# Kernel optimization log

Measured on AMD Instinct MI355X. Metric: run time of the kernel, lower is better.

## Reference

```python
import jax, jax.numpy as jnp
import numpy as np

B, IN, OUT = 1024, 512, 64000
EPS = 1e-12  # matches torch F.normalize eps


def setup_inputs() -> dict:
    key = jax.random.key(0)
    k1, k2, k3 = jax.random.split(key, 3)
    x = jax.random.normal(k1, (B, IN), dtype=jnp.float32)
    label = jax.random.randint(k2, (B,), 0, OUT)
    # xavier_uniform_ for weight [OUT, IN]: limit = sqrt(6 / (fan_in + fan_out))
    limit = float(np.sqrt(6.0 / (IN + OUT)))
    weight = jax.random.uniform(k3, (OUT, IN), dtype=jnp.float32, minval=-limit, maxval=limit)
    s = 50               # python scalar; set via _calculate_para but UNUSED in normfree output
    m = jnp.full((1,), 0.5, dtype=jnp.float32)  # margin
    return {"x": x, "label": label, "weight": weight, "s": s, "m": m}


def reference(x, label, weight, s, m):
    m = m.reshape(())
    cos_m, sin_m = jnp.cos(m), jnp.sin(m)
    # norm of raw input (the 'normfree' scale replacing s)
    norm = jnp.linalg.norm(x, axis=1, keepdims=True)            # [B, 1]
    xn = x / jnp.maximum(norm, EPS)                             # F.normalize(input)
    wn = weight / jnp.maximum(
        jnp.linalg.norm(weight, axis=1, keepdims=True), EPS)    # F.normalize(weight)
    cosine = xn @ wn.T                                          # [B, OUT]
    sine = jnp.sqrt(jnp.clip(1.0 - cosine * cosine, 0.0, None))
    phi = cosine * cos_m - sine * sin_m                         # cos(theta + m)
    # per-sample loop in torch == one-hot substitution only where cosine > 0
    onehot = jax.nn.one_hot(label, OUT, dtype=bool)             # [B, OUT]
    mod_cosine = jnp.where(onehot & (cosine > 0), phi, cosine)
    return norm * mod_cosine, wn
```

## Files before the change

### kernel.cpp

```cpp
#include <hip/hip_runtime.h>
#include <cstdint>

#define EPSN 1e-12f
static constexpr int B_ROWS = 1024;
static constexpr int IN_DIM = 512;
static constexpr int OUT_DIM = 64000;

typedef __attribute__((ext_vector_type(8))) short bf16x8;
typedef __attribute__((ext_vector_type(4))) float f32x4;

__device__ __forceinline__ unsigned short f2bf(float f) {
  uint32_t u = __builtin_bit_cast(uint32_t, f);
  u += 0x7fffu + ((u >> 16) & 1u);
  return (unsigned short)(u >> 16);
}

__device__ __forceinline__ float wave_sum(float v) {
#pragma unroll
  for (int off = 32; off; off >>= 1) v += __shfl_xor(v, off);
  return v;
}

__device__ __forceinline__ void async16(const void* g, void* l) {
  __builtin_amdgcn_global_load_lds((const __attribute__((address_space(1))) uint32_t*)g,
                                   (__attribute__((address_space(3))) uint32_t*)l, 16, 0, 0);
}

__global__ void wnorm_kernel(const float* __restrict__ Wg, float* __restrict__ wnOut,
                             unsigned short* __restrict__ wbf, int useBf) {
  int lane = threadIdx.x & 63;
  int row = blockIdx.x * 4 + (threadIdx.x >> 6);
  const float* src = Wg + (size_t)row * IN_DIM + lane * 8;
  float4 a = *(const float4*)src;
  float4 b = *(const float4*)(src + 4);
  float ss = a.x * a.x;
  ss = fmaf(a.y, a.y, ss); ss = fmaf(a.z, a.z, ss); ss = fmaf(a.w, a.w, ss);
  ss = fmaf(b.x, b.x, ss); ss = fmaf(b.y, b.y, ss); ss = fmaf(b.z, b.z, ss);
  ss = fmaf(b.w, b.w, ss);
  ss = wave_sum(ss);
  float inv = 1.0f / fmaxf(sqrtf(ss), EPSN);
  float4 wa, wb;
  wa.x = a.x * inv; wa.y = a.y * inv; wa.z = a.z * inv; wa.w = a.w * inv;
  wb.x = b.x * inv; wb.y = b.y * inv; wb.z = b.z * inv; wb.w = b.w * inv;
  float* dst = wnOut + (size_t)row * IN_DIM + lane * 8;
  *(float4*)dst = wa;
  *(float4*)(dst + 4) = wb;
  if (useBf) {
    uint4 u;
    u.x = (uint32_t)f2bf(wa.x) | ((uint32_t)f2bf(wa.y) << 16);
    u.y = (uint32_t)f2bf(wa.z) | ((uint32_t)f2bf(wa.w) << 16);
    u.z = (uint32_t)f2bf(wb.x) | ((uint32_t)f2bf(wb.y) << 16);
    u.w = (uint32_t)f2bf(wb.z) | ((uint32_t)f2bf(wb.w) << 16);
    *(uint4*)(wbf + (size_t)row * IN_DIM + lane * 8) = u;
  }
}

__global__ void xprep_kernel(const float* __restrict__ X, float* __restrict__ norms,
                             unsigned short* __restrict__ xbf) {
  int lane = threadIdx.x & 63;
  int row = blockIdx.x * 4 + (threadIdx.x >> 6);
  const float* src = X + (size_t)row * IN_DIM + lane * 8;
  float4 a = *(const float4*)src;
  float4 b = *(const float4*)(src + 4);
  float ss = a.x * a.x;
  ss = fmaf(a.y, a.y, ss); ss = fmaf(a.z, a.z, ss); ss = fmaf(a.w, a.w, ss);
  ss = fmaf(b.x, b.x, ss); ss = fmaf(b.y, b.y, ss); ss = fmaf(b.z, b.z, ss);
  ss = fmaf(b.w, b.w, ss);
  ss = wave_sum(ss);
  if (lane == 0) norms[row] = sqrtf(ss);
  uint4 u;
  u.x = (uint32_t)f2bf(a.x) | ((uint32_t)f2bf(a.y) << 16);
  u.y = (uint32_t)f2bf(a.z) | ((uint32_t)f2bf(a.w) << 16);
  u.z = (uint32_t)f2bf(b.x) | ((uint32_t)f2bf(b.y) << 16);
  u.w = (uint32_t)f2bf(b.z) | ((uint32_t)f2bf(b.w) << 16);
  *(uint4*)(xbf + (size_t)row * IN_DIM + lane * 8) = u;
}

__global__ void labelfix_kernel(const float* __restrict__ X, const int* __restrict__ label,
                                const float* __restrict__ wn, float* __restrict__ fixdot) {
  int lane = threadIdx.x & 63;
  int row = blockIdx.x * 4 + (threadIdx.x >> 6);
  int lab = label[row];
  const float* xs = X + (size_t)row * IN_DIM + lane * 8;
  const float* wsrc = wn + (size_t)lab * IN_DIM + lane * 8;
  float4 xa = *(const float4*)xs, xb = *(const float4*)(xs + 4);
  float4 wa = *(const float4*)wsrc, wb = *(const float4*)(wsrc + 4);
  float d = xa.x * wa.x;
  d = fmaf(xa.y, wa.y, d); d = fmaf(xa.z, wa.z, d); d = fmaf(xa.w, wa.w, d);
  d = fmaf(xb.x, wb.x, d); d = fmaf(xb.y, wb.y, d); d = fmaf(xb.z, wb.z, d);
  d = fmaf(xb.w, wb.w, d);
  d = wave_sum(d);
  if (lane == 0) fixdot[row] = d;
}

template <bool BF16B>
__global__ __launch_bounds__(256, 2) void gemm_epi_kernel(
    const unsigned short* __restrict__ Abf, const unsigned short* __restrict__ Bbf,
    const float* __restrict__ Bf32, const float* __restrict__ norms,
    const float* __restrict__ fixdot, const int* __restrict__ label,
    const float* __restrict__ mArr, float* __restrict__ out0) {
  __shared__ uint4 smem4[1024];
  char* smem = (char*)smem4;

  int t = threadIdx.x;
  int flat = blockIdx.x;
  int xcd = flat & 7;
  int wk = (flat >> 3) + xcd * 500;
  int mT = wk & 7, nT = wk >> 3;
  int rowA0 = mT * 128, rowB0 = nT * 128;

  int lane = t & 63;
  int wm = (t >> 6) >> 1, wn2 = (t >> 6) & 1;
  int rl = lane & 15, sl = lane >> 4;

  f32x4 acc[4][4];
#pragma unroll
  for (int i = 0; i < 4; ++i)
#pragma unroll
    for (int j = 0; j < 4; ++j) acc[i][j] = (f32x4){0.f, 0.f, 0.f, 0.f};

  for (int kk = 0; kk < 16; ++kk) {
    int k0 = kk * 32;
#pragma unroll
    for (int c = 0; c < 2; ++c) {
      int W = (t + c * 256) * 16;
      int line = W >> 7;
      int xx = ((W >> 4) & 7) ^ (line & 7);
      int r = line * 2 + (xx >> 2), s = xx & 3;
      async16(Abf + (size_t)(rowA0 + r) * IN_DIM + k0 + s * 8, smem + W);
    }
    if constexpr (BF16B) {
#pragma unroll
      for (int c = 0; c < 2; ++c) {
        int W = (t + c * 256) * 16;
        int line = W >> 7;
        int xx = ((W >> 4) & 7) ^ (line & 7);
        int r = line * 2 + (xx >> 2), s = xx & 3;
        async16(Bbf + (size_t)(rowB0 + r) * IN_DIM + k0 + s * 8, smem + 8192 + W);
      }
    } else {
#pragma unroll
      for (int c = 0; c < 2; ++c) {
        int blk = t + c * 256;
        int r = blk >> 2, s = blk & 3;
        const float* srcp = Bf32 + (size_t)(rowB0 + r) * IN_DIM + k0 + s * 8;
        float4 f0 = *(const float4*)srcp;
        float4 f1 = *(const float4*)(srcp + 4);
        uint4 u;
        u.x = (uint32_t)f2bf(f0.x) | ((uint32_t)f2bf(f0.y) << 16);
        u.y = (uint32_t)f2bf(f0.z) | ((uint32_t)f2bf(f0.w) << 16);
        u.z = (uint32_t)f2bf(f1.x) | ((uint32_t)f2bf(f1.y) << 16);
        u.w = (uint32_t)f2bf(f1.z) | ((uint32_t)f2bf(f1.w) << 16);
        int off = 8192 + ((r * 64 + s * 16) ^ (((r >> 1) & 7) << 4));
        *(uint4*)(smem + off) = u;
      }
    }
    __syncthreads();
    bf16x8 av[4], bv[4];
#pragma unroll
    for (int i = 0; i < 4; ++i) {
      int r = wm * 64 + i * 16 + rl;
      av[i] = *(const bf16x8*)(smem + ((r * 64 + sl * 16) ^ (((r >> 1) & 7) << 4)));
    }
#pragma unroll
    for (int j = 0; j < 4; ++j) {
      int r = wn2 * 64 + j * 16 + rl;
      bv[j] = *(const bf16x8*)(smem + 8192 + ((r * 64 + sl * 16) ^ (((r >> 1) & 7) << 4)));
    }
#pragma unroll
    for (int i = 0; i < 4; ++i)
#pragma unroll
      for (int j = 0; j < 4; ++j)
        acc[i][j] = __builtin_amdgcn_mfma_f32_16x16x32_bf16(av[i], bv[j], acc[i][j], 0, 0, 0);
    __syncthreads();
  }

  float mm = mArr[0];
  float cm = cosf(mm), sm = sinf(mm);
  int rowb = rowA0 + wm * 64, colb = rowB0 + wn2 * 64;
#pragma unroll
  for (int i = 0; i < 4; ++i) {
    int lab4[4]; float n4[4], f4[4];
#pragma unroll
    for (int q = 0; q < 4; ++q) {
      int R = rowb + i * 16 + sl * 4 + q;
      lab4[q] = label[R];
      n4[q] = norms[R];
      f4[q] = fixdot[R];
    }
#pragma unroll
    for (int j = 0; j < 4; ++j) {
      int Cc = colb + j * 16 + rl;
      f32x4 v = acc[i][j];
#pragma unroll
      for (int q = 0; q < 4; ++q) {
        float val = v[q];
        if (Cc == lab4[q]) {
          float n = n4[q];
          float c = f4[q] / fmaxf(n, EPSN);
          val = (c > 0.f) ? n * (c * cm - sqrtf(fmaxf(1.f - c * c, 0.f)) * sm) : f4[q];
        }
        out0[(size_t)(rowb + i * 16 + sl * 4 + q) * OUT_DIM + Cc] = val;
      }
    }
  }
}

extern "C" void kernel_launch(void* const* d_in, const int* in_sizes, int n_in,
                              void* d_out, int out_size, void* d_ws, size_t ws_size,
                              hipStream_t stream) {
  const float* x = (const float*)d_in[0];
  const int* label = (const int*)d_in[1];
  const float* weight = (const float*)d_in[2];
  const float* mArr = (const float*)d_in[4];

  float* out0 = (float*)d_out;
  float* wnOut = out0 + (size_t)B_ROWS * OUT_DIM;

  char* ws = (char*)d_ws;
  float* norms = (float*)ws;
  float* fixdot = (float*)(ws + 4096);
  unsigned short* xbf = (unsigned short*)(ws + 8192);
  unsigned short* wbf = (unsigned short*)(ws + 8192 + 2ull * B_ROWS * IN_DIM);
  size_t need = 8192 + 2ull * B_ROWS * IN_DIM + 2ull * OUT_DIM * IN_DIM;
  bool useBf = ws_size >= need;

  wnorm_kernel<<<OUT_DIM / 4, 256, 0, stream>>>(weight, wnOut, wbf, useBf ? 1 : 0);
  xprep_kernel<<<B_ROWS / 4, 256, 0, stream>>>(x, norms, xbf);
  labelfix_kernel<<<B_ROWS / 4, 256, 0, stream>>>(x, label, wnOut, fixdot);
  if (useBf)
    gemm_epi_kernel<true><<<4000, 256, 0, stream>>>(xbf, wbf, wnOut, norms, fixdot,
                                                    label, mArr, out0);
  else
    gemm_epi_kernel<false><<<4000, 256, 0, stream>>>(xbf, wbf, wnOut, norms, fixdot,
                                                     label, mArr, out0);
}
```

Before: 210.2 us.

## Double-buffer LDS tiles and widen GEMM block to 128x256 with 8 waves

The GEMM block grows to 512 threads covering a 128x256 output tile, so each A tile is reused across twice as many columns. The bf16 path also double-buffers the LDS tiles, prefetching the next K slice with async global-to-LDS loads while the current slice is multiplied, and syncs with explicit waitcnt and barriers. This aims to hide global load latency and cut redundant A loads, at the cost of three times the LDS and fewer blocks in flight.

After: 223.1 us. 1.06x slower.

```diff
diff --git a/kernel.cpp b/kernel.cpp
--- a/kernel.cpp
+++ b/kernel.cpp
@@ -94,54 +94,101 @@
 }
 
 template <bool BF16B>
-__global__ __launch_bounds__(256, 2) void gemm_epi_kernel(
+__global__ __launch_bounds__(512, 2) void gemm_epi_kernel(
     const unsigned short* __restrict__ Abf, const unsigned short* __restrict__ Bbf,
     const float* __restrict__ Bf32, const float* __restrict__ norms,
     const float* __restrict__ fixdot, const int* __restrict__ label,
     const float* __restrict__ mArr, float* __restrict__ out0) {
-  __shared__ uint4 smem4[1024];
+  __shared__ uint4 smem4[3072];
   char* smem = (char*)smem4;
 
   int t = threadIdx.x;
   int flat = blockIdx.x;
   int xcd = flat & 7;
-  int wk = (flat >> 3) + xcd * 500;
+  int wk = (flat >> 3) + xcd * 250;
   int mT = wk & 7, nT = wk >> 3;
-  int rowA0 = mT * 128, rowB0 = nT * 128;
+  int rowA0 = mT * 128, rowB0 = nT * 256;
 
   int lane = t & 63;
-  int wm = (t >> 6) >> 1, wn2 = (t >> 6) & 1;
+  int wid = t >> 6;
+  int wm = wid >> 2, wn2 = wid & 3;
   int rl = lane & 15, sl = lane >> 4;
 
+  int Wa = t * 16;
+  int lineA = Wa >> 7;
+  int xa = ((Wa >> 4) & 7) ^ (lineA & 7);
+  int rA = lineA * 2 + (xa >> 2), sA = xa & 3;
+  const unsigned short* aSrc = Abf + (size_t)(rowA0 + rA) * IN_DIM + sA * 8;
+
+  int rB[2], sB[2];
+#pragma unroll
+  for (int c = 0; c < 2; ++c) {
+    int W = (t + c * 512) * 16;
+    int line = W >> 7;
+    int xx = ((W >> 4) & 7) ^ (line & 7);
+    rB[c] = line * 2 + (xx >> 2);
+    sB[c] = xx & 3;
+  }
+  const unsigned short* bSrc0 = Bbf + (size_t)(rowB0 + rB[0]) * IN_DIM + sB[0] * 8;
+  const unsigned short* bSrc1 = Bbf + (size_t)(rowB0 + rB[1]) * IN_DIM + sB[1] * 8;
+
   f32x4 acc[4][4];
 #pragma unroll
   for (int i = 0; i < 4; ++i)
 #pragma unroll
     for (int j = 0; j < 4; ++j) acc[i][j] = (f32x4){0.f, 0.f, 0.f, 0.f};
 
-  for (int kk = 0; kk < 16; ++kk) {
-    int k0 = kk * 32;
-#pragma unroll
-    for (int c = 0; c < 2; ++c) {
-      int W = (t + c * 256) * 16;
-      int line = W >> 7;
-      int xx = ((W >> 4) & 7) ^ (line & 7);
-      int r = line * 2 + (xx >> 2), s = xx & 3;
-      async16(Abf + (size_t)(rowA0 + r) * IN_DIM + k0 + s * 8, smem + W);
-    }
-    if constexpr (BF16B) {
+  if constexpr (BF16B) {
+    async16(aSrc, smem + Wa);
+    async16(bSrc0, smem + 16384 + t * 16);
+    async16(bSrc1, smem + 16384 + (t + 512) * 16);
+
+#pragma unroll 1
+    for (int kk = 0; kk < 16; ++kk) {
+      int cur = kk & 1;
+      if (kk < 15) {
+        int k0 = (kk + 1) * 32;
+        int nxt = cur ^ 1;
+        async16(aSrc + k0, smem + nxt * 8192 + Wa);
+        async16(bSrc0 + k0, smem + 16384 + nxt * 16384 + t * 16);
+        async16(bSrc1 + k0, smem + 16384 + nxt * 16384 + (t + 512) * 16);
+        asm volatile("s_waitcnt vmcnt(3)" ::: "memory");
+      } else {
+        asm volatile("s_waitcnt vmcnt(0)" ::: "memory");
+      }
+      __builtin_amdgcn_s_barrier();
+      __builtin_amdgcn_sched_barrier(0);
+
+      const char* aBase = smem + cur * 8192;
+      const char* bBase = smem + 16384 + cur * 16384;
+      bf16x8 av[4], bv[4];
+#pragma unroll
+      for (int i = 0; i < 4; ++i) {
+        int r = wm * 64 + i * 16 + rl;
+        av[i] = *(const bf16x8*)(aBase + ((r * 64 + sl * 16) ^ (((r >> 1) & 7) << 4)));
+      }
+#pragma unroll
+      for (int j = 0; j < 4; ++j) {
+        int r = wn2 * 64 + j * 16 + rl;
+        bv[j] = *(const bf16x8*)(bBase + ((r * 64 + sl * 16) ^ (((r >> 1) & 7) << 4)));
+      }
+#pragma unroll
+      for (int i = 0; i < 4; ++i)
+#pragma unroll
+        for (int j = 0; j < 4; ++j)
+          acc[i][j] = __builtin_amdgcn_mfma_f32_16x16x32_bf16(av[i], bv[j], acc[i][j], 0, 0, 0);
+      asm volatile("s_waitcnt lgkmcnt(0)" ::: "memory");
+      __builtin_amdgcn_s_barrier();
+      __builtin_amdgcn_sched_barrier(0);
+    }
+  } else {
+#pragma unroll 1
+    for (int kk = 0; kk < 16; ++kk) {
+      int k0 = kk * 32;
+      async16(aSrc + k0, smem + Wa);
 #pragma unroll
       for (int c = 0; c < 2; ++c) {
-        int W = (t + c * 256) * 16;
-        int line = W >> 7;
-        int xx = ((W >> 4) & 7) ^ (line & 7);
-        int r = line * 2 + (xx >> 2), s = xx & 3;
-        async16(Bbf + (size_t)(rowB0 + r) * IN_DIM + k0 + s * 8, smem + 8192 + W);
-      }
-    } else {
-#pragma unroll
-      for (int c = 0; c < 2; ++c) {
-        int blk = t + c * 256;
+        int blk = t + c * 512;
         int r = blk >> 2, s = blk & 3;
         const float* srcp = Bf32 + (size_t)(rowB0 + r) * IN_DIM + k0 + s * 8;
         float4 f0 = *(const float4*)srcp;
@@ -151,28 +198,28 @@
         u.y = (uint32_t)f2bf(f0.z) | ((uint32_t)f2bf(f0.w) << 16);
         u.z = (uint32_t)f2bf(f1.x) | ((uint32_t)f2bf(f1.y) << 16);
         u.w = (uint32_t)f2bf(f1.z) | ((uint32_t)f2bf(f1.w) << 16);
-        int off = 8192 + ((r * 64 + s * 16) ^ (((r >> 1) & 7) << 4));
+        int off = 16384 + ((r * 64 + s * 16) ^ (((r >> 1) & 7) << 4));
         *(uint4*)(smem + off) = u;
       }
-    }
-    __syncthreads();
-    bf16x8 av[4], bv[4];
-#pragma unroll
-    for (int i = 0; i < 4; ++i) {
-      int r = wm * 64 + i * 16 + rl;
-      av[i] = *(const bf16x8*)(smem + ((r * 64 + sl * 16) ^ (((r >> 1) & 7) << 4)));
-    }
-#pragma unroll
-    for (int j = 0; j < 4; ++j) {
-      int r = wn2 * 64 + j * 16 + rl;
-      bv[j] = *(const bf16x8*)(smem + 8192 + ((r * 64 + sl * 16) ^ (((r >> 1) & 7) << 4)));
-    }
-#pragma unroll
-    for (int i = 0; i < 4; ++i)
-#pragma unroll
-      for (int j = 0; j < 4; ++j)
-        acc[i][j] = __builtin_amdgcn_mfma_f32_16x16x32_bf16(av[i], bv[j], acc[i][j], 0, 0, 0);
-    __syncthreads();
+      __syncthreads();
+      bf16x8 av[4], bv[4];
+#pragma unroll
+      for (int i = 0; i < 4; ++i) {
+        int r = wm * 64 + i * 16 + rl;
+        av[i] = *(const bf16x8*)(smem + ((r * 64 + sl * 16) ^ (((r >> 1) & 7) << 4)));
+      }
+#pragma unroll
+      for (int j = 0; j < 4; ++j) {
+        int r = wn2 * 64 + j * 16 + rl;
+        bv[j] = *(const bf16x8*)(smem + 16384 + ((r * 64 + sl * 16) ^ (((r >> 1) & 7) << 4)));
+      }
+#pragma unroll
+      for (int i = 0; i < 4; ++i)
+#pragma unroll
+        for (int j = 0; j < 4; ++j)
+          acc[i][j] = __builtin_amdgcn_mfma_f32_16x16x32_bf16(av[i], bv[j], acc[i][j], 0, 0, 0);
+      __syncthreads();
+    }
   }
 
   float mm = mArr[0];
@@ -229,9 +276,9 @@
   xprep_kernel<<<B_ROWS / 4, 256, 0, stream>>>(x, norms, xbf);
   labelfix_kernel<<<B_ROWS / 4, 256, 0, stream>>>(x, label, wnOut, fixdot);
   if (useBf)
-    gemm_epi_kernel<true><<<4000, 256, 0, stream>>>(xbf, wbf, wnOut, norms, fixdot,
+    gemm_epi_kernel<true><<<2000, 512, 0, stream>>>(xbf, wbf, wnOut, norms, fixdot,
                                                     label, mArr, out0);
   else
-    gemm_epi_kernel<false><<<4000, 256, 0, stream>>>(xbf, wbf, wnOut, norms, fixdot,
+    gemm_epi_kernel<false><<<2000, 512, 0, stream>>>(xbf, wbf, wnOut, norms, fixdot,
                                                      label, mArr, out0);
 }
```

## Use 256x256 tiles with 8 waves and a multi-stage async LDS pipeline

Applied to the files above, without the earlier changes.

Replaces the 128x128 single-stage GEMM with a 512-thread, 256x256-tile kernel. It double-buffers 128KB of LDS and issues async global-to-LDS loads three sub-steps ahead, using explicit vmcnt waits and raw s_barriers so memory transfers overlap the MFMA work. It also merges the x-prep and label-fix kernels into one launch. The larger tiles cut global traffic per FLOP but raise register and LDS pressure, and with 1000 blocks each needing 128KB of LDS, occupancy is likely one block per CU.

Measured after the change: 199.0 us. 5.3% less time.

```diff
diff --git a/kernel.cpp b/kernel.cpp
--- a/kernel.cpp
+++ b/kernel.cpp
@@ -55,152 +55,165 @@
   }
 }
 
-__global__ void xprep_kernel(const float* __restrict__ X, float* __restrict__ norms,
-                             unsigned short* __restrict__ xbf) {
+__global__ void prep_kernel(const float* __restrict__ X, const int* __restrict__ label,
+                            const float* __restrict__ wn, float* __restrict__ norms,
+                            float* __restrict__ fixdot, unsigned short* __restrict__ xbf) {
   int lane = threadIdx.x & 63;
   int row = blockIdx.x * 4 + (threadIdx.x >> 6);
   const float* src = X + (size_t)row * IN_DIM + lane * 8;
   float4 a = *(const float4*)src;
   float4 b = *(const float4*)(src + 4);
-  float ss = a.x * a.x;
-  ss = fmaf(a.y, a.y, ss); ss = fmaf(a.z, a.z, ss); ss = fmaf(a.w, a.w, ss);
-  ss = fmaf(b.x, b.x, ss); ss = fmaf(b.y, b.y, ss); ss = fmaf(b.z, b.z, ss);
-  ss = fmaf(b.w, b.w, ss);
-  ss = wave_sum(ss);
-  if (lane == 0) norms[row] = sqrtf(ss);
   uint4 u;
   u.x = (uint32_t)f2bf(a.x) | ((uint32_t)f2bf(a.y) << 16);
   u.y = (uint32_t)f2bf(a.z) | ((uint32_t)f2bf(a.w) << 16);
   u.z = (uint32_t)f2bf(b.x) | ((uint32_t)f2bf(b.y) << 16);
   u.w = (uint32_t)f2bf(b.z) | ((uint32_t)f2bf(b.w) << 16);
   *(uint4*)(xbf + (size_t)row * IN_DIM + lane * 8) = u;
-}
-
-__global__ void labelfix_kernel(const float* __restrict__ X, const int* __restrict__ label,
-                                const float* __restrict__ wn, float* __restrict__ fixdot) {
-  int lane = threadIdx.x & 63;
-  int row = blockIdx.x * 4 + (threadIdx.x >> 6);
+  float ss = a.x * a.x;
+  ss = fmaf(a.y, a.y, ss); ss = fmaf(a.z, a.z, ss); ss = fmaf(a.w, a.w, ss);
+  ss = fmaf(b.x, b.x, ss); ss = fmaf(b.y, b.y, ss); ss = fmaf(b.z, b.z, ss);
+  ss = fmaf(b.w, b.w, ss);
+  ss = wave_sum(ss);
   int lab = label[row];
-  const float* xs = X + (size_t)row * IN_DIM + lane * 8;
   const float* wsrc = wn + (size_t)lab * IN_DIM + lane * 8;
-  float4 xa = *(const float4*)xs, xb = *(const float4*)(xs + 4);
   float4 wa = *(const float4*)wsrc, wb = *(const float4*)(wsrc + 4);
-  float d = xa.x * wa.x;
-  d = fmaf(xa.y, wa.y, d); d = fmaf(xa.z, wa.z, d); d = fmaf(xa.w, wa.w, d);
-  d = fmaf(xb.x, wb.x, d); d = fmaf(xb.y, wb.y, d); d = fmaf(xb.z, wb.z, d);
-  d = fmaf(xb.w, wb.w, d);
+  float d = a.x * wa.x;
+  d = fmaf(a.y, wa.y, d); d = fmaf(a.z, wa.z, d); d = fmaf(a.w, wa.w, d);
+  d = fmaf(b.x, wb.x, d); d = fmaf(b.y, wb.y, d); d = fmaf(b.z, wb.z, d);
+  d = fmaf(b.w, wb.w, d);
   d = wave_sum(d);
-  if (lane == 0) fixdot[row] = d;
+  if (lane == 0) { norms[row] = sqrtf(ss); fixdot[row] = d; }
 }
 
 template <bool BF16B>
-__global__ __launch_bounds__(256, 2) void gemm_epi_kernel(
+__global__ __launch_bounds__(512, 2) void gemm8_kernel(
     const unsigned short* __restrict__ Abf, const unsigned short* __restrict__ Bbf,
     const float* __restrict__ Bf32, const float* __restrict__ norms,
     const float* __restrict__ fixdot, const int* __restrict__ label,
     const float* __restrict__ mArr, float* __restrict__ out0) {
-  __shared__ uint4 smem4[1024];
-  char* smem = (char*)smem4;
-
-  int t = threadIdx.x;
+  __shared__ char smem[131072];
+
+  const int t = threadIdx.x;
   int flat = blockIdx.x;
   int xcd = flat & 7;
-  int wk = (flat >> 3) + xcd * 500;
-  int mT = wk & 7, nT = wk >> 3;
-  int rowA0 = mT * 128, rowB0 = nT * 128;
+  int wk = (flat >> 3) + xcd * 125;
+  int mT = wk & 3, nT = wk >> 2;
+  int rowA0 = mT * 256, rowB0 = nT * 256;
 
   int lane = t & 63;
-  int wm = (t >> 6) >> 1, wn2 = (t >> 6) & 1;
+  int wid = t >> 6;
+  int wm = wid >> 2, wn2 = wid & 3;
   int rl = lane & 15, sl = lane >> 4;
 
-  f32x4 acc[4][4];
-#pragma unroll
-  for (int i = 0; i < 4; ++i)
-#pragma unroll
-    for (int j = 0; j < 4; ++j) acc[i][j] = (f32x4){0.f, 0.f, 0.f, 0.f};
-
-  for (int kk = 0; kk < 16; ++kk) {
-    int k0 = kk * 32;
-#pragma unroll
-    for (int c = 0; c < 2; ++c) {
-      int W = (t + c * 256) * 16;
-      int line = W >> 7;
-      int xx = ((W >> 4) & 7) ^ (line & 7);
-      int r = line * 2 + (xx >> 2), s = xx & 3;
-      async16(Abf + (size_t)(rowA0 + r) * IN_DIM + k0 + s * 8, smem + W);
-    }
+  int r0 = t >> 2, q0 = (t & 3) ^ ((r0 >> 1) & 3);
+  int r1 = (t + 512) >> 2, q1 = ((t + 512) & 3) ^ ((r1 >> 1) & 3);
+  const unsigned short* aP0 = Abf + (size_t)(rowA0 + r0) * IN_DIM + q0 * 8;
+  const unsigned short* aP1 = Abf + (size_t)(rowA0 + r1) * IN_DIM + q1 * 8;
+  const unsigned short* bP0 = Bbf + (size_t)(rowB0 + r0) * IN_DIM + q0 * 8;
+  const unsigned short* bP1 = Bbf + (size_t)(rowB0 + r1) * IN_DIM + q1 * 8;
+  const float* bF0 = Bf32 + (size_t)(rowB0 + r0) * IN_DIM + q0 * 8;
+  const float* bF1 = Bf32 + (size_t)(rowB0 + r1) * IN_DIM + q1 * 8;
+
+  auto issueSub = [&](int sig) {
+    int kt = sig >> 1, s = sig & 1, buf = kt & 1;
+    char* aD = smem + buf * 65536 + s * 16384;
+    char* bD = aD + 32768;
+    int kcol = kt * 64 + s * 32;
+    async16(aP0 + kcol, aD + t * 16);
+    async16(aP1 + kcol, aD + (t + 512) * 16);
     if constexpr (BF16B) {
-#pragma unroll
-      for (int c = 0; c < 2; ++c) {
-        int W = (t + c * 256) * 16;
-        int line = W >> 7;
-        int xx = ((W >> 4) & 7) ^ (line & 7);
-        int r = line * 2 + (xx >> 2), s = xx & 3;
-        async16(Bbf + (size_t)(rowB0 + r) * IN_DIM + k0 + s * 8, smem + 8192 + W);
-      }
+      async16(bP0 + kcol, bD + t * 16);
+      async16(bP1 + kcol, bD + (t + 512) * 16);
     } else {
-#pragma unroll
-      for (int c = 0; c < 2; ++c) {
-        int blk = t + c * 256;
-        int r = blk >> 2, s = blk & 3;
-        const float* srcp = Bf32 + (size_t)(rowB0 + r) * IN_DIM + k0 + s * 8;
-        float4 f0 = *(const float4*)srcp;
-        float4 f1 = *(const float4*)(srcp + 4);
-        uint4 u;
-        u.x = (uint32_t)f2bf(f0.x) | ((uint32_t)f2bf(f0.y) << 16);
-        u.y = (uint32_t)f2bf(f0.z) | ((uint32_t)f2bf(f0.w) << 16);
-        u.z = (uint32_t)f2bf(f1.x) | ((uint32_t)f2bf(f1.y) << 16);
-        u.w = (uint32_t)f2bf(f1.z) | ((uint32_t)f2bf(f1.w) << 16);
-        int off = 8192 + ((r * 64 + s * 16) ^ (((r >> 1) & 7) << 4));
-        *(uint4*)(smem + off) = u;
-      }
-    }
-    __syncthreads();
-    bf16x8 av[4], bv[4];
-#pragma unroll
-    for (int i = 0; i < 4; ++i) {
-      int r = wm * 64 + i * 16 + rl;
-      av[i] = *(const bf16x8*)(smem + ((r * 64 + sl * 16) ^ (((r >> 1) & 7) << 4)));
-    }
-#pragma unroll
-    for (int j = 0; j < 4; ++j) {
-      int r = wn2 * 64 + j * 16 + rl;
-      bv[j] = *(const bf16x8*)(smem + 8192 + ((r * 64 + sl * 16) ^ (((r >> 1) & 7) << 4)));
-    }
-#pragma unroll
-    for (int i = 0; i < 4; ++i)
-#pragma unroll
-      for (int j = 0; j < 4; ++j)
-        acc[i][j] = __builtin_amdgcn_mfma_f32_16x16x32_bf16(av[i], bv[j], acc[i][j], 0, 0, 0);
-    __syncthreads();
+      float4 f0 = *(const float4*)(bF0 + kcol);
+      float4 f1 = *(const float4*)(bF0 + kcol + 4);
+      uint4 u;
+      u.x = (uint32_t)f2bf(f0.x) | ((uint32_t)f2bf(f0.y) << 16);
+      u.y = (uint32_t)f2bf(f0.z) | ((uint32_t)f2bf(f0.w) << 16);
+      u.z = (uint32_t)f2bf(f1.x) | ((uint32_t)f2bf(f1.y) << 16);
+      u.w = (uint32_t)f2bf(f1.z) | ((uint32_t)f2bf(f1.w) << 16);
+      *(uint4*)(bD + t * 16) = u;
+      f0 = *(const float4*)(bF1 + kcol);
+      f1 = *(const float4*)(bF1 + kcol + 4);
+      u.x = (uint32_t)f2bf(f0.x) | ((uint32_t)f2bf(f0.y) << 16);
+      u.y = (uint32_t)f2bf(f0.z) | ((uint32_t)f2bf(f0.w) << 16);
+      u.z = (uint32_t)f2bf(f1.x) | ((uint32_t)f2bf(f1.y) << 16);
+      u.w = (uint32_t)f2bf(f1.z) | ((uint32_t)f2bf(f1.w) << 16);
+      *(uint4*)(bD + (t + 512) * 16) = u;
+    }
+  };
+
+  issueSub(0); issueSub(1); issueSub(2);
+
+  f32x4 acc[8][4];
+#pragma unroll
+  for (int m = 0; m < 8; ++m)
+#pragma unroll
+    for (int n = 0; n < 4; ++n) acc[m][n] = (f32x4){0.f, 0.f, 0.f, 0.f};
+
+#pragma unroll 1
+  for (int sigma = 0; sigma < 16; ++sigma) {
+    int kt = sigma >> 1, s = sigma & 1, buf = kt & 1;
+    if constexpr (BF16B) {
+      int remain = 15 - sigma;
+      __builtin_amdgcn_sched_barrier(0);
+      if (remain >= 2)      asm volatile("s_waitcnt vmcnt(8)" ::: "memory");
+      else if (remain == 1) asm volatile("s_waitcnt vmcnt(4)" ::: "memory");
+      else                  asm volatile("s_waitcnt vmcnt(0)" ::: "memory");
+      __builtin_amdgcn_s_barrier();
+      __builtin_amdgcn_sched_barrier(0);
+    } else {
+      __syncthreads();
+    }
+    const char* aB = smem + buf * 65536 + s * 16384;
+    const char* bB = aB + 32768;
+    bf16x8 av[8], bv[4];
+#pragma unroll
+    for (int m = 0; m < 8; ++m) {
+      int r = wm * 128 + m * 16 + rl;
+      av[m] = *(const bf16x8*)(aB + r * 64 + ((sl ^ ((r >> 1) & 3)) * 16));
+    }
+#pragma unroll
+    for (int n = 0; n < 4; ++n) {
+      int r = wn2 * 64 + n * 16 + rl;
+      bv[n] = *(const bf16x8*)(bB + r * 64 + ((sl ^ ((r >> 1) & 3)) * 16));
+    }
+    if (sigma + 3 <= 15) issueSub(sigma + 3);
+    __builtin_amdgcn_s_setprio(1);
+#pragma unroll
+    for (int n = 0; n < 4; ++n)
+#pragma unroll
+      for (int m = 0; m < 8; ++m)
+        acc[m][n] = __builtin_amdgcn_mfma_f32_16x16x32_bf16(av[m], bv[n], acc[m][n], 0, 0, 0);
+    __builtin_amdgcn_s_setprio(0);
+    if constexpr (BF16B) {
+      __builtin_amdgcn_s_barrier();
+      __builtin_amdgcn_sched_barrier(0);
+    } else {
+      __syncthreads();
+    }
   }
 
   float mm = mArr[0];
   float cm = cosf(mm), sm = sinf(mm);
-  int rowb = rowA0 + wm * 64, colb = rowB0 + wn2 * 64;
-#pragma unroll
-  for (int i = 0; i < 4; ++i) {
-    int lab4[4]; float n4[4], f4[4];
+  int rowb = rowA0 + wm * 128, colb = rowB0 + wn2 * 64;
+#pragma unroll
+  for (int m = 0; m < 8; ++m) {
 #pragma unroll
     for (int q = 0; q < 4; ++q) {
-      int R = rowb + i * 16 + sl * 4 + q;
-      lab4[q] = label[R];
-      n4[q] = norms[R];
-      f4[q] = fixdot[R];
-    }
-#pragma unroll
-    for (int j = 0; j < 4; ++j) {
-      int Cc = colb + j * 16 + rl;
-      f32x4 v = acc[i][j];
-#pragma unroll
-      for (int q = 0; q < 4; ++q) {
-        float val = v[q];
-        if (Cc == lab4[q]) {
-          float n = n4[q];
-          float c = f4[q] / fmaxf(n, EPSN);
-          val = (c > 0.f) ? n * (c * cm - sqrtf(fmaxf(1.f - c * c, 0.f)) * sm) : f4[q];
+      int R = rowb + m * 16 + sl * 4 + q;
+      int lab = label[R];
+      float nv = norms[R], fv = fixdot[R];
+      float* orow = out0 + (size_t)R * OUT_DIM;
+#pragma unroll
+      for (int n = 0; n < 4; ++n) {
+        int Cc = colb + n * 16 + rl;
+        float val = acc[m][n][q];
+        if (Cc == lab) {
+          float c = fv / fmaxf(nv, EPSN);
+          val = (c > 0.f) ? nv * (c * cm - sqrtf(fmaxf(1.f - c * c, 0.f)) * sm) : fv;
         }
-        out0[(size_t)(rowb + i * 16 + sl * 4 + q) * OUT_DIM + Cc] = val;
+        orow[Cc] = val;
       }
     }
   }
@@ -226,12 +239,11 @@
   bool useBf = ws_size >= need;
 
   wnorm_kernel<<<OUT_DIM / 4, 256, 0, stream>>>(weight, wnOut, wbf, useBf ? 1 : 0);
-  xprep_kernel<<<B_ROWS / 4, 256, 0, stream>>>(x, norms, xbf);
-  labelfix_kernel<<<B_ROWS / 4, 256, 0, stream>>>(x, label, wnOut, fixdot);
+  prep_kernel<<<B_ROWS / 4, 256, 0, stream>>>(x, label, wnOut, norms, fixdot, xbf);
   if (useBf)
-    gemm_epi_kernel<true><<<4000, 256, 0, stream>>>(xbf, wbf, wnOut, norms, fixdot,
-                                                    label, mArr, out0);
+    gemm8_kernel<true><<<1000, 512, 0, stream>>>(xbf, wbf, wnOut, norms, fixdot,
+                                                 label, mArr, out0);
   else
-    gemm_epi_kernel<false><<<4000, 256, 0, stream>>>(xbf, wbf, wnOut, norms, fixdot,
-                                                     label, mArr, out0);
-}
+    gemm8_kernel<false><<<1000, 512, 0, stream>>>(xbf, wbf, wnOut, norms, fixdot,
+                                                  label, mArr, out0);
+}
```
